# Performance work log

Hardware: AMD Instinct MI355X
Metric: run time of the kernel (lower is better)

The kernel has to match this reference:

```python
import jax, jax.numpy as jnp
import numpy as np

D_IN = 1024
D_OUT = 1024
N_HEADS = 16
HEAD_DIM = D_OUT // N_HEADS


def setup_inputs() -> dict:
    key = jax.random.key(0)
    ks = jax.random.split(key, 6)
    s = 0.02
    return {
        "x": jax.random.normal(ks[0], (2, 2048, D_IN), dtype=jnp.float32),
        "W_q": jax.random.normal(ks[1], (D_IN, D_OUT), dtype=jnp.float32) * s,
        "W_k": jax.random.normal(ks[2], (D_IN, D_OUT), dtype=jnp.float32) * s,
        "W_v": jax.random.normal(ks[3], (D_IN, D_OUT), dtype=jnp.float32) * s,
        "W_o": jax.random.normal(ks[4], (D_OUT, D_OUT), dtype=jnp.float32) * s,
        "b_o": jax.random.normal(ks[5], (D_OUT,), dtype=jnp.float32) * s,
    }


def reference(x, W_q, W_k, W_v, W_o, b_o):
    B, S, _ = x.shape
    # projections -> [B, H, S, Dh]
    def split_heads(t):
        return t.reshape(B, S, N_HEADS, HEAD_DIM).transpose(0, 2, 1, 3)
    q = split_heads(x @ W_q)
    k = split_heads(x @ W_k)
    v = split_heads(x @ W_v)
    scores = jnp.einsum("bhqd,bhkd->bhqk", q, k)
    causal = jnp.triu(jnp.ones((S, S), dtype=bool), k=1)  # True above diagonal
    scores = jnp.where(causal, -jnp.inf, scores)
    attn = jax.nn.softmax(scores / jnp.sqrt(jnp.float32(HEAD_DIM)), axis=-1)
    ctx = jnp.einsum("bhqk,bhkd->bhqd", attn, v)  # [B,H,S,Dh]
    ctx = ctx.transpose(0, 2, 1, 3).reshape(B, S, D_OUT)
    return ctx @ W_o + b_o
```

## Files before the change

### kernel.cpp

```cpp
#include <hip/hip_runtime.h>
#include <math.h>

typedef unsigned short u16;
typedef unsigned int u32;
typedef short v8s __attribute__((ext_vector_type(8)));
typedef float v4f __attribute__((ext_vector_type(4)));
typedef u16 u16x4v __attribute__((ext_vector_type(4)));

#define S_LEN 2048
#define D_MODEL 1024
#define DH 64
#define BS_ROWS 4096

__device__ __forceinline__ u16 f2bf(float f) {
    union { float f; unsigned int u; } c; c.f = f;
    unsigned int u = c.u;
    unsigned int r = (u + 0x7FFFu + ((u >> 16) & 1u)) >> 16;
    return (u16)r;
}
__device__ __forceinline__ u16 f2bf_fast(float f) {
    return (u16)((__float_as_uint(f) + 0x8000u) >> 16);
}

__device__ __forceinline__ v4f mfma16(v8s a, v8s b, v4f c) {
    return __builtin_amdgcn_mfma_f32_16x16x32_bf16(a, b, c, 0, 0, 0);
}

__device__ __forceinline__ void gl_lds(const u16* g, u16* l) {
    __builtin_amdgcn_global_load_lds(
        (const __attribute__((address_space(1))) void*)g,
        (__attribute__((address_space(3))) void*)l, 16, 0, 0);
}

__global__ __launch_bounds__(256) void cast_x_kernel(const float* __restrict__ x,
                                                     u16* __restrict__ xb, int n4) {
    int i = blockIdx.x * 256 + threadIdx.x;
    if (i < n4) {
        float4 v = ((const float4*)x)[i];
        u16x4v o;
        o[0] = f2bf(v.x); o[1] = f2bf(v.y); o[2] = f2bf(v.z); o[3] = f2bf(v.w);
        ((u16x4v*)xb)[i] = o;
    }
}

__global__ __launch_bounds__(256) void pack_wt_kernel(const float* __restrict__ Wq,
                                                      const float* __restrict__ Wk,
                                                      const float* __restrict__ Wv,
                                                      const float* __restrict__ Wo,
                                                      u16* __restrict__ wqkv,
                                                      u16* __restrict__ wo_t) {
    __shared__ u16 tile[64][72];
    int z = blockIdx.z;
    const float* w = (z == 0) ? Wq : (z == 1) ? Wk : (z == 2) ? Wv : Wo;
    u16* wt = (z < 3) ? (wqkv + (size_t)z * 1024 * 1024) : wo_t;
    int k0 = blockIdx.x * 64, n0 = blockIdx.y * 64;
    int t = threadIdx.x;
    int tr = t >> 4;
    int tc = (t & 15) * 4;
#pragma unroll
    for (int i = 0; i < 4; ++i) {
        int k = tr + 16 * i;
        float4 v = *(const float4*)(w + (size_t)(k0 + k) * 1024 + n0 + tc);
        tile[tc + 0][k] = f2bf(v.x);
        tile[tc + 1][k] = f2bf(v.y);
        tile[tc + 2][k] = f2bf(v.z);
        tile[tc + 3][k] = f2bf(v.w);
    }
    __syncthreads();
#pragma unroll
    for (int i = 0; i < 4; ++i) {
        int n = tr + 16 * i;
        u16x4v o;
        o[0] = tile[n][tc]; o[1] = tile[n][tc + 1];
        o[2] = tile[n][tc + 2]; o[3] = tile[n][tc + 3];
        *(u16x4v*)(wt + (size_t)(n0 + n) * 1024 + k0 + tc) = o;
    }
}

template <int MODE>
__global__ __launch_bounds__(256, 3) void gemm_kernel(
    const u16* __restrict__ A, const u16* __restrict__ Bt,
    const float* __restrict__ bias,
    u16* __restrict__ q_out, u16* __restrict__ k_out, u16* __restrict__ v_out,
    float* __restrict__ out_f32) {
    constexpr int BN = (MODE == 0) ? 128 : 64;
    constexpr int MT = (MODE == 0) ? 4 : 2;
    constexpr int K = 1024;
    __shared__ __align__(16) u16 As[128 * 64];
    __shared__ __align__(16) u16 Bs[BN * 64];
    int tid = threadIdx.x;
    int lane = tid & 63;
    int w = tid >> 6;
    int n16 = lane & 15, quad = lane >> 4;
    int lrow = lane >> 3, lchunk = lane & 7;
    int m0 = blockIdx.y * 128, n0 = blockIdx.x * BN;
    int wm_off = (MODE == 0) ? (w >> 1) * 64 : w * 32;
    int wn_off = (MODE == 0) ? (w & 1) * 64 : 0;

    v4f acc[MT][4];
#pragma unroll
    for (int i = 0; i < MT; ++i)
#pragma unroll
        for (int j = 0; j < 4; ++j) acc[i][j] = v4f{0, 0, 0, 0};

    for (int k0 = 0; k0 < K; k0 += 64) {
#pragma unroll
        for (int i = 0; i < 4; ++i) {
            int r = w * 32 + i * 8 + lrow;
            int gc = lchunk ^ (r & 7);
            gl_lds(A + (size_t)(m0 + r) * K + k0 + gc * 8, As + (w * 32 + i * 8) * 64);
        }
        if (MODE == 0) {
#pragma unroll
            for (int i = 0; i < 4; ++i) {
                int r = w * 32 + i * 8 + lrow;
                int gc = lchunk ^ (r & 7);
                gl_lds(Bt + (size_t)(n0 + r) * K + k0 + gc * 8, Bs + (w * 32 + i * 8) * 64);
            }
        } else {
#pragma unroll
            for (int i = 0; i < 2; ++i) {
                int r = w * 16 + i * 8 + lrow;
                int gc = lchunk ^ (r & 7);
                gl_lds(Bt + (size_t)(n0 + r) * K + k0 + gc * 8, Bs + (w * 16 + i * 8) * 64);
            }
        }
        __syncthreads();
#pragma unroll
        for (int kk = 0; kk < 64; kk += 32) {
            v8s af[MT], bf[4];
#pragma unroll
            for (int mt = 0; mt < MT; ++mt) {
                int ra = wm_off + mt * 16 + n16;
                af[mt] = *(const v8s*)(As + ra * 64 + ((((kk >> 3) + quad) ^ (ra & 7)) << 3));
            }
#pragma unroll
            for (int nt = 0; nt < 4; ++nt) {
                int rb = wn_off + nt * 16 + n16;
                bf[nt] = *(const v8s*)(Bs + rb * 64 + ((((kk >> 3) + quad) ^ (rb & 7)) << 3));
            }
#pragma unroll
            for (int mt = 0; mt < MT; ++mt)
#pragma unroll
                for (int nt = 0; nt < 4; ++nt)
                    acc[mt][nt] = mfma16(af[mt], bf[nt], acc[mt][nt]);
        }
        __syncthreads();
    }

#pragma unroll
    for (int mt = 0; mt < MT; ++mt) {
#pragma unroll
        for (int nt = 0; nt < 4; ++nt) {
            if (MODE == 0) {
                int colb = n0 + wn_off + nt * 16;
                int rowb = m0 + wm_off + mt * 16 + quad * 4;
                int which = colb >> 10;
                int hb = (colb & 1023) >> 6;
                int d = (colb & 63) + n16;
                int b = rowb >> 11, s = rowb & 2047;
                int bh = b * 16 + hb;
                if (which == 0) {
#pragma unroll
                    for (int r = 0; r < 4; ++r)
                        q_out[((size_t)bh * S_LEN + s + r) * DH + d] =
                            f2bf(acc[mt][nt][r] * 0.125f);
                } else if (which == 1) {
#pragma unroll
                    for (int r = 0; r < 4; ++r)
                        k_out[((size_t)bh * S_LEN + s + r) * DH + d] = f2bf(acc[mt][nt][r]);
                } else {
                    u16x4v pk;
#pragma unroll
                    for (int r = 0; r < 4; ++r) pk[r] = f2bf(acc[mt][nt][r]);
                    *(u16x4v*)(v_out + ((size_t)bh * DH + d) * S_LEN + s) = pk;
                }
            } else {
#pragma unroll
                for (int r = 0; r < 4; ++r) {
                    int row = m0 + wm_off + mt * 16 + quad * 4 + r;
                    int col = n0 + nt * 16 + n16;
                    out_f32[(size_t)row * 1024 + col] = acc[mt][nt][r] + bias[col];
                }
            }
        }
    }
}

template <bool DIAG>
__device__ __forceinline__ void attn_step(const u16* __restrict__ ks,
                                          const u16* __restrict__ vs,
                                          u16* __restrict__ pw,
                                          v8s qa0, v8s qa1,
                                          v4f* acc, float* l_r,
                                          int kb, int rowg, int n16, int quad) {
    v4f s[4];
#pragma unroll
    for (int nt = 0; nt < 4; ++nt) {
        int rk = nt * 16 + n16;
        const u16* kr = ks + rk * 64;
        v4f t = v4f{0, 0, 0, 0};
        t = mfma16(qa0, *(const v8s*)(kr + ((quad ^ (rk & 7)) << 3)), t);
        t = mfma16(qa1, *(const v8s*)(kr + (((4 + quad) ^ (rk & 7)) << 3)), t);
        s[nt] = t;
    }
#pragma unroll
    for (int r = 0; r < 4; ++r) {
#pragma unroll
        for (int nt = 0; nt < 4; ++nt) {
            float e = __expf(s[nt][r]);
            if (DIAG) {
                if (kb + nt * 16 + n16 > rowg + r) e = 0.0f;
            }
            l_r[r] += e;
            pw[(quad * 4 + r) * 68 + nt * 16 + n16] = f2bf_fast(e);
        }
    }
    v8s pa0 = *(const v8s*)(pw + n16 * 68 + quad * 8);
    v8s pa1 = *(const v8s*)(pw + n16 * 68 + 32 + quad * 8);
#pragma unroll
    for (int f = 0; f < 4; ++f) {
        int rv = f * 16 + n16;
        const u16* vr = vs + rv * 64;
        acc[f] = mfma16(pa0, *(const v8s*)(vr + ((quad ^ (rv & 7)) << 3)), acc[f]);
        acc[f] = mfma16(pa1, *(const v8s*)(vr + (((4 + quad) ^ (rv & 7)) << 3)), acc[f]);
    }
}

__global__ __launch_bounds__(256, 3) void attn_kernel(const u16* __restrict__ Qg,
                                                      const u16* __restrict__ Kg,
                                                      const u16* __restrict__ Vtg,
                                                      u16* __restrict__ ctx) {
    __shared__ __align__(16) u16 Ks[2][64 * 64];
    __shared__ __align__(16) u16 Vs[2][64 * 64];
    __shared__ __align__(16) u16 Ps[4][16 * 68];

    int i = blockIdx.x;
    int xcd = i & 7;
    int j = i >> 3;
    int bh = xcd * 4 + (j & 3);
    int qt = 31 - (j >> 2);
    int qbase = qt * 64;
    int tid = threadIdx.x;
    int w = tid >> 6;
    int lane = tid & 63;
    int n16 = lane & 15;
    int quad = lane >> 4;
    int lrow = lane >> 3, lchunk = lane & 7;

    const u16* Qb = Qg + (size_t)bh * (S_LEN * DH);
    const u16* Kb = Kg + (size_t)bh * (S_LEN * DH);
    const u16* Vtb = Vtg + (size_t)bh * (S_LEN * DH);
    u16* pw = Ps[w];
    int b = bh >> 4, h = bh & 15;
    int cur = 0;

    auto stage = [&](int kb, int buf) {
#pragma unroll
        for (int i2 = 0; i2 < 2; ++i2) {
            int r = w * 16 + i2 * 8 + lrow;
            int gc = lchunk ^ (r & 7);
            gl_lds(Kb + (size_t)(kb + r) * DH + gc * 8, &Ks[buf][(w * 16 + i2 * 8) * 64]);
            gl_lds(Vtb + (size_t)r * S_LEN + kb + gc * 8, &Vs[buf][(w * 16 + i2 * 8) * 64]);
        }
    };

    int qrow = qbase + w * 16 + n16;
    v8s qa0 = *(const v8s*)(Qb + (size_t)qrow * DH + quad * 8);
    v8s qa1 = *(const v8s*)(Qb + (size_t)qrow * DH + 32 + quad * 8);

    v4f acc[4];
    float l_r[4];
#pragma unroll
    for (int f = 0; f < 4; ++f) acc[f] = v4f{0, 0, 0, 0};
#pragma unroll
    for (int r = 0; r < 4; ++r) l_r[r] = 0.0f;
    int rowg = qbase + w * 16 + quad * 4;
    int nkb = qt + 1;

    stage(0, cur);
    for (int it = 0; it < nkb - 1; ++it) {
        __syncthreads();
        stage((it + 1) * 64, cur ^ 1);
        attn_step<false>(Ks[cur], Vs[cur], pw, qa0, qa1, acc, l_r,
                         it * 64, rowg, n16, quad);
        cur ^= 1;
    }
    __syncthreads();
    attn_step<true>(Ks[cur], Vs[cur], pw, qa0, qa1, acc, l_r,
                    (nkb - 1) * 64, rowg, n16, quad);

#pragma unroll
    for (int r = 0; r < 4; ++r) {
        float l = l_r[r];
        l += __shfl_xor(l, 1);
        l += __shfl_xor(l, 2);
        l += __shfl_xor(l, 4);
        l += __shfl_xor(l, 8);
        float inv = 1.0f / l;
        int srow = qbase + w * 16 + quad * 4 + r;
        size_t base = ((size_t)(b * S_LEN + srow)) * D_MODEL + h * DH;
#pragma unroll
        for (int f = 0; f < 4; ++f)
            ctx[base + f * 16 + n16] = f2bf(acc[f][r] * inv);
    }
}

extern "C" void kernel_launch(void* const* d_in, const int* in_sizes, int n_in,
                              void* d_out, int out_size, void* d_ws, size_t ws_size,
                              hipStream_t stream) {
    const float* x  = (const float*)d_in[0];
    const float* Wq = (const float*)d_in[1];
    const float* Wk = (const float*)d_in[2];
    const float* Wv = (const float*)d_in[3];
    const float* Wo = (const float*)d_in[4];
    const float* bo = (const float*)d_in[5];
    float* out = (float*)d_out;

    char* ws = (char*)d_ws;
    u16* x_bf = (u16*)ws;   ws += (size_t)BS_ROWS * D_MODEL * 2;
    u16* wqkv = (u16*)ws;   ws += (size_t)3 * D_MODEL * D_MODEL * 2;
    u16* wo_t = (u16*)ws;   ws += (size_t)D_MODEL * D_MODEL * 2;
    u16* qbuf = (u16*)ws;   ws += (size_t)BS_ROWS * D_MODEL * 2;
    u16* kbuf = (u16*)ws;   ws += (size_t)BS_ROWS * D_MODEL * 2;
    u16* vtbuf = (u16*)ws;  ws += (size_t)BS_ROWS * D_MODEL * 2;
    u16* ctx = (u16*)ws;    ws += (size_t)BS_ROWS * D_MODEL * 2;

    cast_x_kernel<<<4096, 256, 0, stream>>>(x, x_bf, BS_ROWS * D_MODEL / 4);
    pack_wt_kernel<<<dim3(16, 16, 4), 256, 0, stream>>>(Wq, Wk, Wv, Wo, wqkv, wo_t);

    gemm_kernel<0><<<dim3(24, 32), 256, 0, stream>>>(x_bf, wqkv, nullptr,
                                                     qbuf, kbuf, vtbuf, nullptr);
    attn_kernel<<<1024, 256, 0, stream>>>(qbuf, kbuf, vtbuf, ctx);
    gemm_kernel<1><<<dim3(16, 32), 256, 0, stream>>>(ctx, wo_t, bo,
                                                     nullptr, nullptr, nullptr, out);
}
```

Measured before the change: 184.5 us.

## Fuse prep kernels, use exp2 with folded log2e, transpose score MFMA layout

The x cast and weight transpose kernels are merged into one launch to save a kernel launch. The attention inner loop now swaps the MFMA operands so each lane holds scores for a single query row. This lets the row sum live in one scalar and lets P be written as packed bf16 pairs into a swizzled LDS tile without padding. The softmax scale now includes log2(e) and the exponential uses the hardware exp2, and the occupancy hint is raised from 3 to 4 blocks per CU. The risks are register pressure at the higher occupancy target and correctness of the new swizzle and diagonal mask indexing.

```diff
diff --git a/kernel.cpp b/kernel.cpp
--- a/kernel.cpp
+++ b/kernel.cpp
@@ -6,11 +6,20 @@
 typedef short v8s __attribute__((ext_vector_type(8)));
 typedef float v4f __attribute__((ext_vector_type(4)));
 typedef u16 u16x4v __attribute__((ext_vector_type(4)));
+typedef u32 u32x2 __attribute__((ext_vector_type(2)));
 
 #define S_LEN 2048
 #define D_MODEL 1024
 #define DH 64
 #define BS_ROWS 4096
+
+#define QSCALE 0.1803368801111204f
+
+#if __has_builtin(__builtin_amdgcn_exp2f)
+#define EXP2(x) __builtin_amdgcn_exp2f(x)
+#else
+#define EXP2(x) __expf(0.6931471805599453f * (x))
+#endif
 
 __device__ __forceinline__ u16 f2bf(float f) {
     union { float f; unsigned int u; } c; c.f = f;
@@ -18,8 +27,10 @@
     unsigned int r = (u + 0x7FFFu + ((u >> 16) & 1u)) >> 16;
     return (u16)r;
 }
-__device__ __forceinline__ u16 f2bf_fast(float f) {
-    return (u16)((__float_as_uint(f) + 0x8000u) >> 16);
+__device__ __forceinline__ u32 pack2bf(float a, float b) {
+    u32 ua = __float_as_uint(a) + 0x8000u;
+    u32 ub = __float_as_uint(b) + 0x8000u;
+    return (ua >> 16) | (ub & 0xFFFF0000u);
 }
 
 __device__ __forceinline__ v4f mfma16(v8s a, v8s b, v4f c) {
@@ -32,29 +43,31 @@
         (__attribute__((address_space(3))) void*)l, 16, 0, 0);
 }
 
-__global__ __launch_bounds__(256) void cast_x_kernel(const float* __restrict__ x,
-                                                     u16* __restrict__ xb, int n4) {
-    int i = blockIdx.x * 256 + threadIdx.x;
-    if (i < n4) {
+__global__ __launch_bounds__(256) void prep_kernel(const float* __restrict__ x,
+                                                   const float* __restrict__ Wq,
+                                                   const float* __restrict__ Wk,
+                                                   const float* __restrict__ Wv,
+                                                   const float* __restrict__ Wo,
+                                                   u16* __restrict__ xb,
+                                                   u16* __restrict__ wqkv,
+                                                   u16* __restrict__ wo_t) {
+    __shared__ u16 tile[64][72];
+    int blk = blockIdx.x;
+    int t = threadIdx.x;
+    if (blk < 4096) {
+        int i = blk * 256 + t;
         float4 v = ((const float4*)x)[i];
         u16x4v o;
         o[0] = f2bf(v.x); o[1] = f2bf(v.y); o[2] = f2bf(v.z); o[3] = f2bf(v.w);
         ((u16x4v*)xb)[i] = o;
-    }
-}
-
-__global__ __launch_bounds__(256) void pack_wt_kernel(const float* __restrict__ Wq,
-                                                      const float* __restrict__ Wk,
-                                                      const float* __restrict__ Wv,
-                                                      const float* __restrict__ Wo,
-                                                      u16* __restrict__ wqkv,
-                                                      u16* __restrict__ wo_t) {
-    __shared__ u16 tile[64][72];
-    int z = blockIdx.z;
+        return;
+    }
+    int pb = blk - 4096;
+    int z = pb >> 8;
+    pb &= 255;
     const float* w = (z == 0) ? Wq : (z == 1) ? Wk : (z == 2) ? Wv : Wo;
     u16* wt = (z < 3) ? (wqkv + (size_t)z * 1024 * 1024) : wo_t;
-    int k0 = blockIdx.x * 64, n0 = blockIdx.y * 64;
-    int t = threadIdx.x;
+    int k0 = (pb & 15) * 64, n0 = (pb >> 4) * 64;
     int tr = t >> 4;
     int tc = (t & 15) * 4;
 #pragma unroll
@@ -164,7 +177,7 @@
 #pragma unroll
                     for (int r = 0; r < 4; ++r)
                         q_out[((size_t)bh * S_LEN + s + r) * DH + d] =
-                            f2bf(acc[mt][nt][r] * 0.125f);
+                            f2bf(acc[mt][nt][r] * QSCALE);
                 } else if (which == 1) {
 #pragma unroll
                     for (int r = 0; r < 4; ++r)
@@ -192,32 +205,39 @@
                                           const u16* __restrict__ vs,
                                           u16* __restrict__ pw,
                                           v8s qa0, v8s qa1,
-                                          v4f* acc, float* l_r,
-                                          int kb, int rowg, int n16, int quad) {
-    v4f s[4];
+                                          v4f* acc, float& l,
+                                          int n16, int quad, int wq) {
+    v4f st[4];
 #pragma unroll
     for (int nt = 0; nt < 4; ++nt) {
         int rk = nt * 16 + n16;
         const u16* kr = ks + rk * 64;
         v4f t = v4f{0, 0, 0, 0};
-        t = mfma16(qa0, *(const v8s*)(kr + ((quad ^ (rk & 7)) << 3)), t);
-        t = mfma16(qa1, *(const v8s*)(kr + (((4 + quad) ^ (rk & 7)) << 3)), t);
-        s[nt] = t;
-    }
-#pragma unroll
-    for (int r = 0; r < 4; ++r) {
-#pragma unroll
-        for (int nt = 0; nt < 4; ++nt) {
-            float e = __expf(s[nt][r]);
+        t = mfma16(*(const v8s*)(kr + ((quad ^ (rk & 7)) << 3)), qa0, t);
+        t = mfma16(*(const v8s*)(kr + (((4 + quad) ^ (rk & 7)) << 3)), qa1, t);
+        st[nt] = t;
+    }
+    int h = n16 & 7;
+    u16* prow = pw + n16 * 64;
+#pragma unroll
+    for (int nt = 0; nt < 4; ++nt) {
+        float e[4];
+#pragma unroll
+        for (int r = 0; r < 4; ++r) {
+            float v = EXP2(st[nt][r]);
             if (DIAG) {
-                if (kb + nt * 16 + n16 > rowg + r) e = 0.0f;
-            }
-            l_r[r] += e;
-            pw[(quad * 4 + r) * 68 + nt * 16 + n16] = f2bf_fast(e);
-        }
-    }
-    v8s pa0 = *(const v8s*)(pw + n16 * 68 + quad * 8);
-    v8s pa1 = *(const v8s*)(pw + n16 * 68 + 32 + quad * 8);
+                if (nt * 16 + quad * 4 + r > wq) v = 0.0f;
+            }
+            e[r] = v;
+            l += v;
+        }
+        u32x2 pk;
+        pk[0] = pack2bf(e[0], e[1]);
+        pk[1] = pack2bf(e[2], e[3]);
+        *(u32x2*)(prow + (((2 * nt + (quad >> 1)) ^ h) << 3) + (quad & 1) * 4) = pk;
+    }
+    v8s pa0 = *(const v8s*)(prow + ((quad ^ h) << 3));
+    v8s pa1 = *(const v8s*)(prow + (((4 + quad) ^ h) << 3));
 #pragma unroll
     for (int f = 0; f < 4; ++f) {
         int rv = f * 16 + n16;
@@ -227,13 +247,13 @@
     }
 }
 
-__global__ __launch_bounds__(256, 3) void attn_kernel(const u16* __restrict__ Qg,
+__global__ __launch_bounds__(256, 4) void attn_kernel(const u16* __restrict__ Qg,
                                                       const u16* __restrict__ Kg,
                                                       const u16* __restrict__ Vtg,
                                                       u16* __restrict__ ctx) {
     __shared__ __align__(16) u16 Ks[2][64 * 64];
     __shared__ __align__(16) u16 Vs[2][64 * 64];
-    __shared__ __align__(16) u16 Ps[4][16 * 68];
+    __shared__ __align__(16) u16 Ps[4][16 * 64];
 
     int i = blockIdx.x;
     int xcd = i & 7;
@@ -270,34 +290,28 @@
     v8s qa1 = *(const v8s*)(Qb + (size_t)qrow * DH + 32 + quad * 8);
 
     v4f acc[4];
-    float l_r[4];
 #pragma unroll
     for (int f = 0; f < 4; ++f) acc[f] = v4f{0, 0, 0, 0};
-#pragma unroll
-    for (int r = 0; r < 4; ++r) l_r[r] = 0.0f;
-    int rowg = qbase + w * 16 + quad * 4;
+    float l = 0.0f;
+    int wq = w * 16 + n16;
     int nkb = qt + 1;
 
     stage(0, cur);
     for (int it = 0; it < nkb - 1; ++it) {
         __syncthreads();
         stage((it + 1) * 64, cur ^ 1);
-        attn_step<false>(Ks[cur], Vs[cur], pw, qa0, qa1, acc, l_r,
-                         it * 64, rowg, n16, quad);
+        attn_step<false>(Ks[cur], Vs[cur], pw, qa0, qa1, acc, l, n16, quad, wq);
         cur ^= 1;
     }
     __syncthreads();
-    attn_step<true>(Ks[cur], Vs[cur], pw, qa0, qa1, acc, l_r,
-                    (nkb - 1) * 64, rowg, n16, quad);
-
+    attn_step<true>(Ks[cur], Vs[cur], pw, qa0, qa1, acc, l, n16, quad, wq);
+
+    l += __shfl_xor(l, 16);
+    l += __shfl_xor(l, 32);
 #pragma unroll
     for (int r = 0; r < 4; ++r) {
-        float l = l_r[r];
-        l += __shfl_xor(l, 1);
-        l += __shfl_xor(l, 2);
-        l += __shfl_xor(l, 4);
-        l += __shfl_xor(l, 8);
-        float inv = 1.0f / l;
+        float lq = __shfl(l, quad * 4 + r);
+        float inv = 1.0f / lq;
         int srow = qbase + w * 16 + quad * 4 + r;
         size_t base = ((size_t)(b * S_LEN + srow)) * D_MODEL + h * DH;
 #pragma unroll
@@ -326,8 +340,7 @@
     u16* vtbuf = (u16*)ws;  ws += (size_t)BS_ROWS * D_MODEL * 2;
     u16* ctx = (u16*)ws;    ws += (size_t)BS_ROWS * D_MODEL * 2;
 
-    cast_x_kernel<<<4096, 256, 0, stream>>>(x, x_bf, BS_ROWS * D_MODEL / 4);
-    pack_wt_kernel<<<dim3(16, 16, 4), 256, 0, stream>>>(Wq, Wk, Wv, Wo, wqkv, wo_t);
+    prep_kernel<<<5120, 256, 0, stream>>>(x, Wq, Wk, Wv, Wo, x_bf, wqkv, wo_t);
 
     gemm_kernel<0><<<dim3(24, 32), 256, 0, stream>>>(x_bf, wqkv, nullptr,
                                                      qbuf, kbuf, vtbuf, nullptr);
```

After: 169.9 us. -7.9%, faster.
